# Kernel tuning notes

Measured on AMD Instinct MI355X. Metric: run time of the kernel, lower is better.

The kernel has to match this reference:

```python
import jax, jax.numpy as jnp
import numpy as np

B, I, O, E, K = 32768, 256, 128, 8, 4


def _layernorm(h, g, b, eps=1e-5):
    mu = h.mean(-1, keepdims=True)
    var = h.var(-1, keepdims=True)
    return (h - mu) * jax.lax.rsqrt(var + eps) * g + b


def setup_inputs():
    key = jax.random.key(0)
    ks = iter(jax.random.split(key, 40))
    def w(shape, scale=0.02):
        return jax.random.normal(next(ks), shape, dtype=jnp.float32) * scale
    inp = {
        'x': jax.random.normal(next(ks), (B, I), dtype=jnp.float32),
        'modality_id': jax.random.randint(next(ks), (B,), 0, 3, dtype=jnp.int32),
        # experts 0-1: Linear-ReLU-Linear (stacked over leading expert dim)
        'A_W1': w((2, O, I)), 'A_b1': w((2, O)), 'A_W2': w((2, O, O)), 'A_b2': w((2, O)),
        # experts 2-3: Linear-Tanh-BatchNorm1d(eval)-Linear
        'B_W1': w((2, O, I)), 'B_b1': w((2, O)),
        'B_g': jnp.ones((2, O), jnp.float32), 'B_be': jnp.zeros((2, O), jnp.float32),
        'B_W2': w((2, O, O)), 'B_b2': w((2, O)),
        # experts 4-5: Conv1d(1->4,k3,p1)-Flatten-Linear-GELU
        'C_cw': w((2, 4, 1, 3), 0.1), 'C_cb': w((2, 4)),
        'C_W': w((2, O, 4 * I)), 'C_b': w((2, O)),
        # experts 6-7: Linear-SiLU-LayerNorm-Linear
        'D_W1': w((2, O, I)), 'D_b1': w((2, O)),
        'D_g': jnp.ones((2, O), jnp.float32), 'D_be': jnp.zeros((2, O), jnp.float32),
        'D_W2': w((2, O, O)), 'D_b2': w((2, O)),
        # shared expert: Linear-ReLU-LayerNorm-Linear (dropout off in eval)
        'S_W1': w((O, I)), 'S_b1': w((O,)),
        'S_g': jnp.ones((O,), jnp.float32), 'S_be': jnp.zeros((O,), jnp.float32),
        'S_W2': w((O, O)), 'S_b2': w((O,)),
        # gate: Linear(I+1 -> I//2)-Tanh-Linear(-> E)
        'G_W1': w((I // 2, I + 1)), 'G_b1': w((I // 2,)),
        'G_W2': w((E, I // 2)), 'G_b2': w((E,)),
    }
    return inp


def _forward(x, modality_id, A_W1, A_b1, A_W2, A_b2, B_W1, B_b1, B_g, B_be, B_W2, B_b2,
             C_cw, C_cb, C_W, C_b, D_W1, D_b1, D_g, D_be, D_W2, D_b2,
             S_W1, S_b1, S_g, S_be, S_W2, S_b2, G_W1, G_b1, G_W2, G_b2):
    Bsz = x.shape[0]
    mod = modality_id.astype(x.dtype)[:, None]
    gate_in = jnp.concatenate([x, mod], axis=-1)                 # [B, I+1]
    gh = jnp.tanh(gate_in @ G_W1.T + G_b1)
    logits = jnp.clip((gh @ G_W2.T + G_b2) / 0.7, -10.0, 10.0)   # [B, E]
    topv, topi = jax.lax.top_k(logits, K)
    topw = jax.nn.softmax(topv, axis=-1)                          # [B, K]

    # experts 0-1
    hA = jax.nn.relu(jnp.einsum('bi,eoi->beo', x, A_W1) + A_b1)
    outA = jnp.einsum('beo,epo->bep', hA, A_W2) + A_b2
    # experts 2-3 (BatchNorm eval: running mean 0, var 1)
    hB = jnp.tanh(jnp.einsum('bi,eoi->beo', x, B_W1) + B_b1)
    hB = hB * jax.lax.rsqrt(jnp.asarray(1.0 + 1e-5, x.dtype)) * B_g + B_be
    outB = jnp.einsum('beo,epo->bep', hB, B_W2) + B_b2
    # experts 4-5
    xc = x[:, None, :]                                            # [B,1,I]
    outC = []
    for e in range(2):
        conv = jax.lax.conv_general_dilated(
            xc, C_cw[e], (1,), [(1, 1)],
            dimension_numbers=('NCH', 'OIH', 'NCH')) + C_cb[e][None, :, None]  # [B,4,I]
        flat = conv.reshape(Bsz, 4 * x.shape[1])
        outC.append(jax.nn.gelu(flat @ C_W[e].T + C_b[e], approximate=False))
    outC = jnp.stack(outC, axis=1)
    # experts 6-7
    hD = jax.nn.silu(jnp.einsum('bi,eoi->beo', x, D_W1) + D_b1)
    hD = _layernorm(hD, D_g, D_be)
    outD = jnp.einsum('beo,epo->bep', hD, D_W2) + D_b2

    expert_outputs = jnp.concatenate([outA, outB, outC, outD], axis=1)  # [B,E,O]
    picked = jnp.take_along_axis(expert_outputs, topi[:, :, None], axis=1)  # [B,K,O]
    private = jnp.sum(topw[:, :, None] * picked, axis=1)                # [B,O]

    hS = jax.nn.relu(x @ S_W1.T + S_b1)
    hS = _layernorm(hS, S_g, S_be)
    shared = hS @ S_W2.T + S_b2                                         # [B,O]

    usage = jax.nn.softmax(logits, axis=-1).mean(0)                     # [E]
    ideal = jnp.full_like(usage, 1.0 / E)
    # F.kl_div(log(usage+1e-10), ideal, reduction='batchmean') with N=E
    aux = jnp.mean(ideal * (jnp.log(ideal) - jnp.log(usage + 1e-10)))
    return shared, private, aux


def reference(x, modality_id, A_W1, A_b1, A_W2, A_b2, B_W1, B_b1, B_g, B_be, B_W2, B_b2,
              C_cw, C_cb, C_W, C_b, D_W1, D_b1, D_g, D_be, D_W2, D_b2,
              S_W1, S_b1, S_g, S_be, S_W2, S_b2, G_W1, G_b1, G_W2, G_b2):
    return _forward(x, modality_id, A_W1, A_b1, A_W2, A_b2, B_W1, B_b1, B_g, B_be, B_W2, B_b2,
                    C_cw, C_cb, C_W, C_b, D_W1, D_b1, D_g, D_be, D_W2, D_b2,
                    S_W1, S_b1, S_g, S_be, S_W2, S_b2, G_W1, G_b1, G_W2, G_b2)
```

## Files before the change

kernel.cpp:

```cpp
#include <hip/hip_runtime.h>
#include <hip/hip_bf16.h>
#include <math.h>

typedef __attribute__((ext_vector_type(8))) short short8;
typedef __attribute__((ext_vector_type(4))) float f32x4;
typedef __attribute__((ext_vector_type(4))) unsigned short us4;

#define MFMA16(a,b,c) __builtin_amdgcn_mfma_f32_16x16x32_bf16((a),(b),(c),0,0,0)

#define OFF_W1CAT   0u
#define OFF_W2CAT   589824u
#define OFF_B1      950272u
#define OFF_B2      954880u
#define OFF_LNG     958464u
#define OFF_LNB     960000u
#define OFF_BSC     961536u
#define OFF_BBI     962560u
#define OFF_USAGE   963584u
#define OFF_W8      963712u
#define OFF_W1T     2012288u
#define OFF_GW1HF   2143872u
#define OFF_GW1LF   2209408u
#define OFF_CNT     2274944u
#define OFF_LIST    2275008u

#define DELTA 3e-4f

__device__ __forceinline__ unsigned short f2bf(float f) {
  union { float f; unsigned u; } v; v.f = f;
  return (unsigned short)((v.u + 0x7fffu + ((v.u >> 16) & 1u)) >> 16);
}
__device__ __forceinline__ float bf2f(unsigned short b) {
  union { unsigned u; float f; } v; v.u = ((unsigned)b) << 16; return v.f;
}
__device__ __forceinline__ float frcp(float x) { return __builtin_amdgcn_rcpf(x); }
__device__ __forceinline__ float ftanh(float x) {
  float ax = fabsf(x);
  float t = __expf(-2.f * ax);
  float r = (1.f - t) * frcp(1.f + t);
  return copysignf(r, x);
}
__device__ __forceinline__ float ftanh_acc(float x) {
  float ax = fabsf(x);
  float t = __expf(-2.f * ax);
  float r = (1.f - t) / (1.f + t);
  return copysignf(r, x);
}
__device__ __forceinline__ float fsilu(float x) {
  return x * frcp(1.f + __expf(-x));
}
__device__ __forceinline__ float fgelu(float x) {
  float ax = fabsf(x) * 0.70710678118654752f;
  float t = frcp(fmaf(0.3275911f, ax, 1.f));
  float p = fmaf(t, 1.061405429f, -1.453152027f);
  p = fmaf(t, p, 1.421413741f);
  p = fmaf(t, p, -0.284496736f);
  p = fmaf(t, p, 0.254829592f);
  p *= t;
  float erfv = copysignf(fmaf(-p, __expf(-ax * ax), 1.f), x);
  return 0.5f * x * (1.f + erfv);
}
__device__ __forceinline__ void gld_lds16(const void* g, void* l) {
  __builtin_amdgcn_global_load_lds(
      (const __attribute__((address_space(1))) void*)g,
      (__attribute__((address_space(3))) void*)l, 16, 0, 0);
}

__global__ __launch_bounds__(256) void prep_kernel(
    const float* __restrict__ A_W1, const float* __restrict__ A_b1,
    const float* __restrict__ A_W2, const float* __restrict__ A_b2,
    const float* __restrict__ B_W1, const float* __restrict__ B_b1,
    const float* __restrict__ B_g,  const float* __restrict__ B_be,
    const float* __restrict__ B_W2, const float* __restrict__ B_b2,
    const float* __restrict__ C_cw, const float* __restrict__ C_cb,
    const float* __restrict__ C_W,  const float* __restrict__ C_b,
    const float* __restrict__ D_W1, const float* __restrict__ D_b1,
    const float* __restrict__ D_g,  const float* __restrict__ D_be,
    const float* __restrict__ D_W2, const float* __restrict__ D_b2,
    const float* __restrict__ S_W1, const float* __restrict__ S_b1,
    const float* __restrict__ S_g,  const float* __restrict__ S_be,
    const float* __restrict__ S_W2, const float* __restrict__ S_b2,
    const float* __restrict__ G_W1,
    unsigned short* __restrict__ W1cat, unsigned short* __restrict__ W2cat,
    float* __restrict__ W1T,
    unsigned short* __restrict__ GW1HF, unsigned short* __restrict__ GW1LF,
    float* __restrict__ b1cat, float* __restrict__ b2cat,
    float* __restrict__ lng, float* __restrict__ lnb,
    float* __restrict__ bsc, float* __restrict__ bbi,
    float* __restrict__ usage)
{
  int tid = blockIdx.x * 256 + threadIdx.x;
  if (tid < 294912) {
    int g = tid >> 15, rem = tid & 32767;
    int j = rem & 7, lane = (rem >> 3) & 63, nt = (rem >> 9) & 7, ks = rem >> 12;
    int p = nt * 16 + (lane & 15);
    int k = ks * 32 + (lane >> 4) * 8 + j;
    int src = p * 256 + k;
    float v;
    if (g < 2)      v = A_W1[g * 32768 + src];
    else if (g < 4) v = B_W1[(g - 2) * 32768 + src];
    else if (g < 6) {
      int e = g - 4;
      v = 0.f;
      for (int c = 0; c < 4; ++c)
        for (int jj = 0; jj < 3; ++jj) {
          int h = k + 1 - jj;
          if (h >= 0 && h < 256)
            v += C_cw[e*12 + c*3 + jj] * C_W[e*131072 + p*1024 + c*256 + h];
        }
    }
    else if (g < 8) v = D_W1[(g - 6) * 32768 + src];
    else            v = S_W1[src];
    W1cat[tid] = f2bf(v);
    return;
  }
  tid -= 294912;
  if (tid < 114688) {
    int g = tid >> 14, rem = tid & 16383;
    int j = rem & 7, lane = (rem >> 3) & 63, nt = (rem >> 9) & 7, ks = rem >> 12;
    int p = nt * 16 + (lane & 15);
    int k = ks * 32 + (lane >> 4) * 8 + j;
    int src = p * 128 + k;
    float v;
    if (g < 2)      v = A_W2[g * 16384 + src];
    else if (g < 4) v = B_W2[(g - 2) * 16384 + src];
    else if (g < 6) v = D_W2[(g - 4) * 16384 + src];
    else            v = S_W2[src];
    W2cat[tid] = f2bf(v);
    return;
  }
  tid -= 114688;
  if (tid < 32896) {
    int k = tid / 128, o = tid % 128;
    W1T[tid] = G_W1[o * 257 + k];
    return;
  }
  tid -= 32896;
  if (tid < 32768) {
    int j = tid & 7, lane = (tid >> 3) & 63, nt = (tid >> 9) & 7, ks = tid >> 12;
    int o = nt * 16 + (lane & 15);
    int k = ks * 32 + (lane >> 4) * 8 + j;
    float v = G_W1[o * 257 + k];
    unsigned short h = f2bf(v);
    GW1HF[tid] = h;
    GW1LF[tid] = f2bf(v - bf2f(h));
    return;
  }
  tid -= 32768;
  if (tid < 1152) {
    int g = tid / 128, p = tid % 128;
    float v;
    if (g < 2)      v = A_b1[tid];
    else if (g < 4) v = B_b1[p + (g - 2) * 128];
    else if (g < 6) v = C_b[(g - 4) * 128 + p];
    else if (g < 8) v = D_b1[p + (g - 6) * 128];
    else            v = S_b1[p];
    b1cat[tid] = v;
    return;
  }
  tid -= 1152;
  if (tid < 896) {
    int g = tid / 128, p = tid % 128;
    float v;
    if (g < 2)      v = A_b2[tid];
    else if (g < 4) v = B_b2[p + (g - 2) * 128];
    else if (g < 6) v = D_b2[p + (g - 4) * 128];
    else            v = S_b2[p];
    b2cat[tid] = v;
    return;
  }
  tid -= 896;
  if (tid < 768) {
    if (tid < 384) {
      int j = tid / 128, p = tid % 128;
      lng[tid] = (j < 2) ? D_g[tid] : S_g[p];
    } else {
      int q = tid - 384; int j = q / 128, p = q % 128;
      lnb[q] = (j < 2) ? D_be[q] : S_be[p];
    }
    return;
  }
  tid -= 768;
  if (tid < 512) {
    if (tid < 256) bsc[tid] = B_g[tid];
    else           bbi[tid - 256] = B_be[tid - 256];
    return;
  }
  tid -= 512;
  if (tid < 8) usage[tid] = 0.f;
}

__global__ __launch_bounds__(256) void prep2_kernel(
    const float* __restrict__ C_cw_unused, const float* __restrict__ C_cb,
    const float* __restrict__ C_W, float* __restrict__ b1cat, int* __restrict__ cnt)
{
  int tid = blockIdx.x * 256 + threadIdx.x;
  if (tid == 0) *cnt = 0;
  int e = tid >> 9, rem = tid & 511;
  int p = rem >> 2, c = rem & 3;
  const float4* row = (const float4*)(C_W + e*131072 + p*1024 + c*256);
  float s = 0.f;
  for (int q = 0; q < 64; ++q) {
    float4 v = row[q];
    s += v.x + v.y + v.z + v.w;
  }
  atomicAdd(&b1cat[(4 + e) * 128 + p], C_cb[e * 4 + c] * s);
}

__global__ __launch_bounds__(512, 4) void gate_fast_kernel(
    const float* __restrict__ x, const int* __restrict__ modality,
    const unsigned short* __restrict__ GW1HF, const unsigned short* __restrict__ GW1LF,
    const float* __restrict__ G_W1, const float* __restrict__ G_b1,
    const float* __restrict__ G_W2, const float* __restrict__ G_b2,
    float* __restrict__ w8full, float* __restrict__ usage,
    int* __restrict__ cnt, int* __restrict__ list)
{
  __shared__ float gh[64][132];
  __shared__ float lgs[64][9];
  const int tid = threadIdx.x;
  const int wv = tid >> 6, lane = tid & 63;
  const int l15 = lane & 15, l4 = lane >> 4;
  const int tg = wv >> 1, half = wv & 1;
  const int tb = blockIdx.x * 64;
  const int tw = tb + tg * 16;

  const short8* srcH = (const short8*)GW1HF;
  const short8* srcL = (const short8*)GW1LF;

  short8 XH[8], XL[8];
#pragma unroll
  for (int ks = 0; ks < 8; ++ks) {
    const float* xr = x + (size_t)(tw + l15) * 256 + ks * 32 + l4 * 8;
    float4 u = *(const float4*)xr, v = *(const float4*)(xr + 4);
    float xv[8] = {u.x, u.y, u.z, u.w, v.x, v.y, v.z, v.w};
    short8 hh, ll;
#pragma unroll
    for (int j2 = 0; j2 < 8; ++j2) {
      unsigned short h = f2bf(xv[j2]);
      hh[j2] = (short)h;
      ll[j2] = (short)f2bf(xv[j2] - bf2f(h));
    }
    XH[ks] = hh; XL[ks] = ll;
  }

  f32x4 zero = {0.f, 0.f, 0.f, 0.f};
  f32x4 acc[4];
#pragma unroll
  for (int n = 0; n < 4; ++n) acc[n] = zero;
#pragma unroll
  for (int ks = 0; ks < 8; ++ks) {
#pragma unroll
    for (int n = 0; n < 4; ++n) {
      int fi = ks * 512 + (half * 4 + n) * 64 + lane;
      short8 bh = srcH[fi];
      short8 bl = srcL[fi];
      acc[n] = MFMA16(XH[ks], bh, acc[n]);
      acc[n] = MFMA16(XH[ks], bl, acc[n]);
      acc[n] = MFMA16(XL[ks], bh, acc[n]);
    }
  }
  float mf[4];
#pragma unroll
  for (int r = 0; r < 4; ++r) mf[r] = (float)modality[tw + l4 * 4 + r];
#pragma unroll
  for (int n = 0; n < 4; ++n) {
    int o = (half * 4 + n) * 16 + l15;
    float wm = G_W1[o * 257 + 256];
    float b = G_b1[o];
#pragma unroll
    for (int r = 0; r < 4; ++r)
      gh[tg * 16 + l4 * 4 + r][o] = ftanh_acc(fmaf(mf[r], wm, acc[n][r]) + b);
  }
  __syncthreads();

  {
    int t2 = tid >> 3, e2 = tid & 7;
    float lg = 0.f;
    for (int o2 = 0; o2 < 128; ++o2)
      lg = fmaf(gh[t2][o2], G_W2[e2 * 128 + o2], lg);
    float s = (lg + G_b2[e2]) / 0.7f;
    lgs[t2][e2] = fminf(fmaxf(s, -10.f), 10.f);
  }
  __syncthreads();

  if (wv == 0) {
    int token = tb + lane;
    float v[8];
#pragma unroll
    for (int e = 0; e < 8; ++e) v[e] = lgs[lane][e];
    float tv[5]; int ti[5]; unsigned msk = 0;
    for (int kk = 0; kk < 5; ++kk) {
      float best = -1e30f; int bi = 0;
      for (int e = 0; e < 8; ++e)
        if (!((msk >> e) & 1u) && v[e] > best) { best = v[e]; bi = e; }
      tv[kk] = best; ti[kk] = bi; msk |= 1u << bi;
    }
    float uw[8];
#pragma unroll
    for (int e = 0; e < 8; ++e) uw[e] = 0.f;
    if (tv[3] - tv[4] < DELTA) {
      int idx = atomicAdd(cnt, 1);
      list[idx] = token;
    } else {
      float mx = tv[0], den = 0.f, wk4[4];
#pragma unroll
      for (int kk = 0; kk < 4; ++kk) { wk4[kk] = expf(tv[kk] - mx); den += wk4[kk]; }
#pragma unroll
      for (int e = 0; e < 8; ++e) {
        float val = 0.f;
#pragma unroll
        for (int kk = 0; kk < 4; ++kk) if (ti[kk] == e) val = wk4[kk] / den;
        w8full[(size_t)token * 8 + e] = val;
      }
      float dall = 0.f, pe[8];
#pragma unroll
      for (int e = 0; e < 8; ++e) { pe[e] = expf(v[e] - mx); dall += pe[e]; }
#pragma unroll
      for (int e = 0; e < 8; ++e) uw[e] = pe[e] / dall;
    }
    for (int m = 1; m <= 32; m <<= 1)
#pragma unroll
      for (int e = 0; e < 8; ++e) uw[e] += __shfl_xor(uw[e], m);
    if (lane == 0)
      for (int e = 0; e < 8; ++e) atomicAdd(usage + e, uw[e]);
  }
}

__global__ __launch_bounds__(256) void gate_slow_kernel(
    const float* __restrict__ x, const int* __restrict__ modality,
    const float* __restrict__ W1T, const float* __restrict__ G_b1,
    const float* __restrict__ G_W2, const float* __restrict__ G_b2,
    const int* __restrict__ cnt, const int* __restrict__ list,
    float* __restrict__ w8full, float* __restrict__ usage)
{
  __shared__ float w1l[32896];
  __shared__ float w2l[8][132];
  __shared__ float xs[4][2][256];
  __shared__ float gh[4][2][128];
  const int n = *cnt;
  if (blockIdx.x * 8 >= n) return;

  for (int idx = threadIdx.x; idx < 8224; idx += 256)
    ((float4*)w1l)[idx] = ((const float4*)W1T)[idx];
  for (int idx = threadIdx.x; idx < 1024; idx += 256)
    w2l[idx >> 7][idx & 127] = G_W2[idx];
  __syncthreads();

  const int wvl = threadIdx.x >> 6, lane = threadIdx.x & 63;
  for (int i0 = blockIdx.x * 8 + wvl * 2; i0 < n; i0 += 2048) {
    const bool v1 = (i0 + 1) < n;
    const int T0 = __builtin_amdgcn_readfirstlane(list[i0]);
    const int T1 = __builtin_amdgcn_readfirstlane(v1 ? list[i0 + 1] : list[i0]);
#pragma unroll
    for (int q = 0; q < 4; ++q) {
      xs[wvl][0][q * 64 + lane] = x[(size_t)T0 * 256 + q * 64 + lane];
      xs[wvl][1][q * 64 + lane] = x[(size_t)T1 * 256 + q * 64 + lane];
    }
    float a0 = 0.f, a1 = 0.f, c0 = 0.f, c1 = 0.f;
#pragma unroll 8
    for (int k = 0; k < 256; ++k) {
      float w0 = w1l[k * 128 + lane];
      float w1 = w1l[k * 128 + 64 + lane];
      float x0 = xs[wvl][0][k];
      float x1 = xs[wvl][1][k];
      a0 = fmaf(x0, w0, a0);
      a1 = fmaf(x0, w1, a1);
      c0 = fmaf(x1, w0, c0);
      c1 = fmaf(x1, w1, c1);
    }
    {
      float xm0 = (float)modality[T0];
      float xm1 = (float)modality[T1];
      float w0 = w1l[256 * 128 + lane];
      float w1 = w1l[256 * 128 + 64 + lane];
      a0 = fmaf(xm0, w0, a0);
      a1 = fmaf(xm0, w1, a1);
      c0 = fmaf(xm1, w0, c0);
      c1 = fmaf(xm1, w1, c1);
    }
    gh[wvl][0][lane]      = (float)tanh((double)(a0 + G_b1[lane]));
    gh[wvl][0][64 + lane] = (float)tanh((double)(a1 + G_b1[64 + lane]));
    gh[wvl][1][lane]      = (float)tanh((double)(c0 + G_b1[lane]));
    gh[wvl][1][64 + lane] = (float)tanh((double)(c1 + G_b1[64 + lane]));
    float lg = 0.f;
    if (lane < 16) {
      int tt2 = lane >> 3, ee = lane & 7;
      for (int o = 0; o < 128; ++o)
        lg = fmaf(gh[wvl][tt2][o], w2l[ee][o], lg);
    }
    float v[8];
#pragma unroll
    for (int e = 0; e < 8; ++e) v[e] = __shfl(lg, (lane & 8) + e);
    if (lane == 0 || (lane == 8 && v1)) {
      const int T = (lane == 0) ? T0 : T1;
#pragma unroll
      for (int e = 0; e < 8; ++e)
        v[e] = fminf(fmaxf((v[e] + G_b2[e]) / 0.7f, -10.f), 10.f);
      float tv[4]; int ti[4]; unsigned msk = 0;
      for (int kk = 0; kk < 4; ++kk) {
        float best = -1e30f; int bi = 0;
        for (int e = 0; e < 8; ++e)
          if (!((msk >> e) & 1u) && v[e] > best) { best = v[e]; bi = e; }
        tv[kk] = best; ti[kk] = bi; msk |= 1u << bi;
      }
      float mx = tv[0], den = 0.f, wk4[4];
#pragma unroll
      for (int kk = 0; kk < 4; ++kk) { wk4[kk] = expf(tv[kk] - mx); den += wk4[kk]; }
#pragma unroll
      for (int e = 0; e < 8; ++e) {
        float val = 0.f;
#pragma unroll
        for (int kk = 0; kk < 4; ++kk) if (ti[kk] == e) val = wk4[kk] / den;
        w8full[(size_t)T * 8 + e] = val;
      }
      float dall = 0.f, pe[8];
#pragma unroll
      for (int e = 0; e < 8; ++e) { pe[e] = expf(v[e] - mx); dall += pe[e]; }
      for (int e = 0; e < 8; ++e) atomicAdd(usage + e, pe[e] / dall);
    }
  }
}

__global__ __launch_bounds__(512, 2) void moe_kernel(
    const float* __restrict__ x,
    const unsigned short* __restrict__ W1cat, const unsigned short* __restrict__ W2cat,
    const float* __restrict__ b1cat, const float* __restrict__ b2cat,
    const float* __restrict__ lng, const float* __restrict__ lnb,
    const float* __restrict__ bsc, const float* __restrict__ bbi,
    const float* __restrict__ w8full, float* __restrict__ out)
{
  __shared__ unsigned char smem[131072];
  short8* W1L = (short8*)smem;
  short8* W2L = (short8*)(smem + 65536);
  unsigned char* HS = smem + 98304 + (threadIdx.x >> 6) * 4096;

  const int tid = threadIdx.x;
  const int wv = tid >> 6, lane = tid & 63;
  const int l15 = lane & 15, l4 = lane >> 4;
  const int tb = blockIdx.x * 128 + wv * 16;

  short8 A[8];
#pragma unroll
  for (int ks = 0; ks < 8; ++ks) {
    const float* xr = x + (size_t)(tb + l15) * 256 + ks * 32 + l4 * 8;
    float4 u = *(const float4*)xr, v = *(const float4*)(xr + 4);
    short8 a;
    a[0]=(short)f2bf(u.x); a[1]=(short)f2bf(u.y); a[2]=(short)f2bf(u.z); a[3]=(short)f2bf(u.w);
    a[4]=(short)f2bf(v.x); a[5]=(short)f2bf(v.y); a[6]=(short)f2bf(v.z); a[7]=(short)f2bf(v.w);
    A[ks] = a;
  }

  f32x4 zero = {0.f, 0.f, 0.f, 0.f};
  f32x4 pacc[8];
#pragma unroll
  for (int nt = 0; nt < 8; ++nt) pacc[nt] = zero;
  const float RS = 1.0f / sqrtf(1.0f + 1e-5f);

  for (int g = 0; g < 9; ++g) {
    const int type = (g < 2) ? 0 : (g < 4) ? 1 : (g < 6) ? 2 : (g < 8) ? 3 : 4;
    const int g2 = (g < 4) ? g : ((g == 8) ? 6 : g - 2);

    __syncthreads();
    {
      const char* W1g = (const char*)W1cat + (size_t)g * 65536;
      const char* W2g = (const char*)W2cat + (size_t)g2 * 32768;
      char* W1Lb = (char*)smem;
      char* W2Lb = (char*)smem + 65536;
      const int wb = wv * 1024;
#pragma unroll
      for (int i = 0; i < 8; ++i) {
        int off = i * 8192 + wb;
        gld_lds16(W1g + off + lane * 16, W1Lb + off);
      }
#pragma unroll
      for (int i = 0; i < 4; ++i) {
        int off = i * 8192 + wb;
        gld_lds16(W2g + off + lane * 16, W2Lb + off);
      }
      asm volatile("s_waitcnt vmcnt(0)" ::: "memory");
    }
    __syncthreads();

    f32x4 acc[8];
#pragma unroll
    for (int nt = 0; nt < 8; ++nt) acc[nt] = zero;
#pragma unroll
    for (int ks = 0; ks < 8; ++ks)
#pragma unroll
      for (int nt = 0; nt < 8; ++nt)
        acc[nt] = MFMA16(A[ks], W1L[(ks * 8 + nt) * 64 + lane], acc[nt]);

    const float* b1 = b1cat + g * 128;

    if (type == 2) {
#pragma unroll
      for (int r = 0; r < 4; ++r) {
        float wv_ = w8full[(size_t)(tb + l4 * 4 + r) * 8 + g];
#pragma unroll
        for (int nt = 0; nt < 8; ++nt) {
          float h = fgelu(acc[nt][r] + b1[nt * 16 + l15]);
          pacc[nt][r] += wv_ * h;
        }
      }
      continue;
    }
#pragma unroll
    for (int r = 0; r < 4; ++r)
#pragma unroll
      for (int nt = 0; nt < 8; ++nt) {
        float h = acc[nt][r] + b1[nt * 16 + l15];
        if (type == 0)      h = fmaxf(h, 0.f);
        else if (type == 1) {
          int col = (g - 2) * 128 + nt * 16 + l15;
          h = ftanh(h) * RS * bsc[col] + bbi[col];
        }
        else if (type == 3) h = fsilu(h);
        else                h = fmaxf(h, 0.f);
        acc[nt][r] = h;
      }
    if (type >= 3) {
      int li = (type == 4) ? 2 : (g - 6);
#pragma unroll
      for (int r = 0; r < 4; ++r) {
        float s1 = 0.f, s2 = 0.f;
#pragma unroll
        for (int nt = 0; nt < 8; ++nt) { float h = acc[nt][r]; s1 += h; s2 += h * h; }
        for (int m = 1; m <= 8; m <<= 1) { s1 += __shfl_xor(s1, m); s2 += __shfl_xor(s2, m); }
        float mu = s1 * (1.f / 128.f);
        float var = s2 * (1.f / 128.f) - mu * mu;
        float sc = __builtin_amdgcn_rsqf(var + 1e-5f);
#pragma unroll
        for (int nt = 0; nt < 8; ++nt) {
          int col = nt * 16 + l15;
          acc[nt][r] = (acc[nt][r] - mu) * sc * lng[li * 128 + col] + lnb[li * 128 + col];
        }
      }
    }
#pragma unroll
    for (int r = 0; r < 4; ++r) {
      int row = l4 * 4 + r;
#pragma unroll
      for (int nt = 0; nt < 8; ++nt) {
        int bytecol = (nt * 16 + l15) * 2;
        int addr = row * 256 + ((((bytecol >> 4) ^ (row & 7)) << 4) | (bytecol & 15));
        *(unsigned short*)(HS + addr) = f2bf(acc[nt][r]);
      }
    }
    short8 a2[4];
#pragma unroll
    for (int ks = 0; ks < 4; ++ks) {
      int ar = l15 * 256 + ((((ks * 4 + l4) ^ (l15 & 7)) << 4));
      a2[ks] = *(const short8*)(HS + ar);
    }
    f32x4 acc2[8];
#pragma unroll
    for (int nt = 0; nt < 8; ++nt) acc2[nt] = zero;
#pragma unroll
    for (int ks = 0; ks < 4; ++ks)
#pragma unroll
      for (int nt = 0; nt < 8; ++nt)
        acc2[nt] = MFMA16(a2[ks], W2L[(ks * 8 + nt) * 64 + lane], acc2[nt]);

    const float* b2 = b2cat + g2 * 128;
    if (type == 4) {
#pragma unroll
      for (int r = 0; r < 4; ++r) {
        int token = tb + l4 * 4 + r;
#pragma unroll
        for (int nt = 0; nt < 8; ++nt)
          out[(size_t)token * 128 + nt * 16 + l15] = acc2[nt][r] + b2[nt * 16 + l15];
      }
    } else {
#pragma unroll
      for (int r = 0; r < 4; ++r) {
        float wv_ = w8full[(size_t)(tb + l4 * 4 + r) * 8 + g];
#pragma unroll
        for (int nt = 0; nt < 8; ++nt)
          pacc[nt][r] += wv_ * (acc2[nt][r] + b2[nt * 16 + l15]);
      }
    }
  }
#pragma unroll
  for (int r = 0; r < 4; ++r) {
    int token = tb + l4 * 4 + r;
#pragma unroll
    for (int nt = 0; nt < 8; ++nt)
      out[4194304 + (size_t)token * 128 + nt * 16 + l15] = pacc[nt][r];
  }
}

__global__ void aux_kernel(const float* __restrict__ usage, float* __restrict__ out) {
  if (threadIdx.x == 0 && blockIdx.x == 0) {
    float a = 0.f;
    for (int e = 0; e < 8; ++e) {
      float u = usage[e] * (1.0f / 32768.0f);
      a += 0.125f * (logf(0.125f) - logf(u + 1e-10f));
    }
    out[8388608] = a * 0.125f;
  }
}

extern "C" void kernel_launch(void* const* d_in, const int* in_sizes, int n_in,
                              void* d_out, int out_size, void* d_ws, size_t ws_size,
                              hipStream_t stream) {
  (void)in_sizes; (void)n_in; (void)out_size; (void)ws_size;
  const float* x    = (const float*)d_in[0];
  const int*   mod  = (const int*)d_in[1];
  const float* A_W1 = (const float*)d_in[2];
  const float* A_b1 = (const float*)d_in[3];
  const float* A_W2 = (const float*)d_in[4];
  const float* A_b2 = (const float*)d_in[5];
  const float* B_W1 = (const float*)d_in[6];
  const float* B_b1 = (const float*)d_in[7];
  const float* B_g  = (const float*)d_in[8];
  const float* B_be = (const float*)d_in[9];
  const float* B_W2 = (const float*)d_in[10];
  const float* B_b2 = (const float*)d_in[11];
  const float* C_cw = (const float*)d_in[12];
  const float* C_cb = (const float*)d_in[13];
  const float* C_W  = (const float*)d_in[14];
  const float* C_b  = (const float*)d_in[15];
  const float* D_W1 = (const float*)d_in[16];
  const float* D_b1 = (const float*)d_in[17];
  const float* D_g  = (const float*)d_in[18];
  const float* D_be = (const float*)d_in[19];
  const float* D_W2 = (const float*)d_in[20];
  const float* D_b2 = (const float*)d_in[21];
  const float* S_W1 = (const float*)d_in[22];
  const float* S_b1 = (const float*)d_in[23];
  const float* S_g  = (const float*)d_in[24];
  const float* S_be = (const float*)d_in[25];
  const float* S_W2 = (const float*)d_in[26];
  const float* S_b2 = (const float*)d_in[27];
  const float* G_W1 = (const float*)d_in[28];
  const float* G_b1 = (const float*)d_in[29];
  const float* G_W2 = (const float*)d_in[30];
  const float* G_b2 = (const float*)d_in[31];

  char* ws = (char*)d_ws;
  unsigned short* W1cat = (unsigned short*)(ws + OFF_W1CAT);
  unsigned short* W2cat = (unsigned short*)(ws + OFF_W2CAT);
  float* W1T    = (float*)(ws + OFF_W1T);
  unsigned short* GW1HF = (unsigned short*)(ws + OFF_GW1HF);
  unsigned short* GW1LF = (unsigned short*)(ws + OFF_GW1LF);
  float* b1cat  = (float*)(ws + OFF_B1);
  float* b2cat  = (float*)(ws + OFF_B2);
  float* lng    = (float*)(ws + OFF_LNG);
  float* lnb    = (float*)(ws + OFF_LNB);
  float* bsc    = (float*)(ws + OFF_BSC);
  float* bbi    = (float*)(ws + OFF_BBI);
  float* usage  = (float*)(ws + OFF_USAGE);
  float* w8full = (float*)(ws + OFF_W8);
  int*   cnt    = (int*)(ws + OFF_CNT);
  int*   list   = (int*)(ws + OFF_LIST);
  float* out    = (float*)d_out;

  prep_kernel<<<1870, 256, 0, stream>>>(A_W1, A_b1, A_W2, A_b2, B_W1, B_b1, B_g, B_be,
      B_W2, B_b2, C_cw, C_cb, C_W, C_b, D_W1, D_b1, D_g, D_be, D_W2, D_b2,
      S_W1, S_b1, S_g, S_be, S_W2, S_b2, G_W1,
      W1cat, W2cat, W1T, GW1HF, GW1LF, b1cat, b2cat, lng, lnb, bsc, bbi, usage);
  prep2_kernel<<<4, 256, 0, stream>>>(C_cw, C_cb, C_W, b1cat, cnt);
  gate_fast_kernel<<<512, 512, 0, stream>>>(x, mod, GW1HF, GW1LF, G_W1, G_b1,
      G_W2, G_b2, w8full, usage, cnt, list);
  gate_slow_kernel<<<256, 256, 0, stream>>>(x, mod, W1T, G_b1, G_W2, G_b2,
      cnt, list, w8full, usage);
  moe_kernel<<<256, 512, 0, stream>>>(x, W1cat, W2cat, b1cat, b2cat, lng, lnb,
      bsc, bbi, w8full, out);
  aux_kernel<<<1, 64, 0, stream>>>(usage, out);
}
```

Before: 214.0 us.

## Split output columns across wave pairs and read W2 straight from global

Each block now handles 64 tokens instead of 128, and two waves share each 16-token tile by splitting the 128 output columns in half. The grid doubles to 512 blocks, and LDS use drops from 128KB to 80KB because W2 is no longer staged in shared memory and is read directly from global memory. The aim is more blocks per GPU and fewer registers per wave. The cost is extra block-wide barriers for the LayerNorm partial sums and for the hidden-tile exchange, plus W1 being staged twice as often per token overall.

```diff
diff --git a/kernel.cpp b/kernel.cpp
--- a/kernel.cpp
+++ b/kernel.cpp
@@ -429,15 +429,16 @@
     const float* __restrict__ bsc, const float* __restrict__ bbi,
     const float* __restrict__ w8full, float* __restrict__ out)
 {
-  __shared__ unsigned char smem[131072];
-  short8* W1L = (short8*)smem;
-  short8* W2L = (short8*)(smem + 65536);
-  unsigned char* HS = smem + 98304 + (threadIdx.x >> 6) * 4096;
-
+  __shared__ unsigned char smem[81920];
   const int tid = threadIdx.x;
   const int wv = tid >> 6, lane = tid & 63;
   const int l15 = lane & 15, l4 = lane >> 4;
-  const int tb = blockIdx.x * 128 + wv * 16;
+  const int t = wv >> 1, half = wv & 1;
+  const int tb = blockIdx.x * 64 + t * 16;
+  unsigned char* HS = smem + 65536 + t * 4096;
+  float* part = (float*)HS;
+  const short8* W1L = (const short8*)smem;
+  const short8* W2f = (const short8*)W2cat;
 
   short8 A[8];
 #pragma unroll
@@ -451,9 +452,9 @@
   }
 
   f32x4 zero = {0.f, 0.f, 0.f, 0.f};
-  f32x4 pacc[8];
-#pragma unroll
-  for (int nt = 0; nt < 8; ++nt) pacc[nt] = zero;
+  f32x4 pacc[4];
+#pragma unroll
+  for (int n = 0; n < 4; ++n) pacc[n] = zero;
   const float RS = 1.0f / sqrtf(1.0f + 1e-5f);
 
   for (int g = 0; g < 9; ++g) {
@@ -463,32 +464,23 @@
     __syncthreads();
     {
       const char* W1g = (const char*)W1cat + (size_t)g * 65536;
-      const char* W2g = (const char*)W2cat + (size_t)g2 * 32768;
-      char* W1Lb = (char*)smem;
-      char* W2Lb = (char*)smem + 65536;
-      const int wb = wv * 1024;
 #pragma unroll
       for (int i = 0; i < 8; ++i) {
-        int off = i * 8192 + wb;
-        gld_lds16(W1g + off + lane * 16, W1Lb + off);
-      }
-#pragma unroll
-      for (int i = 0; i < 4; ++i) {
-        int off = i * 8192 + wb;
-        gld_lds16(W2g + off + lane * 16, W2Lb + off);
+        int off = wv * 8192 + i * 1024;
+        gld_lds16(W1g + off + lane * 16, (char*)smem + off);
       }
       asm volatile("s_waitcnt vmcnt(0)" ::: "memory");
     }
     __syncthreads();
 
-    f32x4 acc[8];
-#pragma unroll
-    for (int nt = 0; nt < 8; ++nt) acc[nt] = zero;
+    f32x4 acc[4];
+#pragma unroll
+    for (int n = 0; n < 4; ++n) acc[n] = zero;
 #pragma unroll
     for (int ks = 0; ks < 8; ++ks)
 #pragma unroll
-      for (int nt = 0; nt < 8; ++nt)
-        acc[nt] = MFMA16(A[ks], W1L[(ks * 8 + nt) * 64 + lane], acc[nt]);
+      for (int n = 0; n < 4; ++n)
+        acc[n] = MFMA16(A[ks], W1L[(ks * 8 + half * 4 + n) * 64 + lane], acc[n]);
 
     const float* b1 = b1cat + g * 128;
 
@@ -497,9 +489,10 @@
       for (int r = 0; r < 4; ++r) {
         float wv_ = w8full[(size_t)(tb + l4 * 4 + r) * 8 + g];
 #pragma unroll
-        for (int nt = 0; nt < 8; ++nt) {
-          float h = fgelu(acc[nt][r] + b1[nt * 16 + l15]);
-          pacc[nt][r] += wv_ * h;
+        for (int n = 0; n < 4; ++n) {
+          int col = (half * 4 + n) * 16 + l15;
+          float h = fgelu(acc[n][r] + b1[col]);
+          pacc[n][r] += wv_ * h;
         }
       }
       continue;
@@ -507,59 +500,75 @@
 #pragma unroll
     for (int r = 0; r < 4; ++r)
 #pragma unroll
-      for (int nt = 0; nt < 8; ++nt) {
-        float h = acc[nt][r] + b1[nt * 16 + l15];
+      for (int n = 0; n < 4; ++n) {
+        int col = (half * 4 + n) * 16 + l15;
+        float h = acc[n][r] + b1[col];
         if (type == 0)      h = fmaxf(h, 0.f);
-        else if (type == 1) {
-          int col = (g - 2) * 128 + nt * 16 + l15;
-          h = ftanh(h) * RS * bsc[col] + bbi[col];
-        }
+        else if (type == 1) h = ftanh(h) * RS * bsc[(g - 2) * 128 + col] + bbi[(g - 2) * 128 + col];
         else if (type == 3) h = fsilu(h);
         else                h = fmaxf(h, 0.f);
-        acc[nt][r] = h;
+        acc[n][r] = h;
       }
     if (type >= 3) {
       int li = (type == 4) ? 2 : (g - 6);
+      float s1h[4], s2h[4];
 #pragma unroll
       for (int r = 0; r < 4; ++r) {
         float s1 = 0.f, s2 = 0.f;
 #pragma unroll
-        for (int nt = 0; nt < 8; ++nt) { float h = acc[nt][r]; s1 += h; s2 += h * h; }
+        for (int n = 0; n < 4; ++n) { float h = acc[n][r]; s1 += h; s2 += h * h; }
         for (int m = 1; m <= 8; m <<= 1) { s1 += __shfl_xor(s1, m); s2 += __shfl_xor(s2, m); }
+        s1h[r] = s1; s2h[r] = s2;
+      }
+      if (l15 == 0) {
+#pragma unroll
+        for (int r = 0; r < 4; ++r) {
+          part[half * 32 + (l4 * 4 + r)] = s1h[r];
+          part[half * 32 + 16 + (l4 * 4 + r)] = s2h[r];
+        }
+      }
+      __syncthreads();
+#pragma unroll
+      for (int r = 0; r < 4; ++r) {
+        int row = l4 * 4 + r;
+        float s1 = part[row] + part[32 + row];
+        float s2 = part[16 + row] + part[48 + row];
         float mu = s1 * (1.f / 128.f);
         float var = s2 * (1.f / 128.f) - mu * mu;
         float sc = __builtin_amdgcn_rsqf(var + 1e-5f);
 #pragma unroll
-        for (int nt = 0; nt < 8; ++nt) {
-          int col = nt * 16 + l15;
-          acc[nt][r] = (acc[nt][r] - mu) * sc * lng[li * 128 + col] + lnb[li * 128 + col];
+        for (int n = 0; n < 4; ++n) {
+          int col = (half * 4 + n) * 16 + l15;
+          acc[n][r] = (acc[n][r] - mu) * sc * lng[li * 128 + col] + lnb[li * 128 + col];
         }
       }
+      __syncthreads();
     }
 #pragma unroll
     for (int r = 0; r < 4; ++r) {
       int row = l4 * 4 + r;
 #pragma unroll
-      for (int nt = 0; nt < 8; ++nt) {
-        int bytecol = (nt * 16 + l15) * 2;
+      for (int n = 0; n < 4; ++n) {
+        int bytecol = ((half * 4 + n) * 16 + l15) * 2;
         int addr = row * 256 + ((((bytecol >> 4) ^ (row & 7)) << 4) | (bytecol & 15));
-        *(unsigned short*)(HS + addr) = f2bf(acc[nt][r]);
-      }
-    }
+        *(unsigned short*)(HS + addr) = f2bf(acc[n][r]);
+      }
+    }
+    __syncthreads();
     short8 a2[4];
 #pragma unroll
     for (int ks = 0; ks < 4; ++ks) {
       int ar = l15 * 256 + ((((ks * 4 + l4) ^ (l15 & 7)) << 4));
       a2[ks] = *(const short8*)(HS + ar);
     }
-    f32x4 acc2[8];
-#pragma unroll
-    for (int nt = 0; nt < 8; ++nt) acc2[nt] = zero;
+    f32x4 acc2[4];
+#pragma unroll
+    for (int n = 0; n < 4; ++n) acc2[n] = zero;
 #pragma unroll
     for (int ks = 0; ks < 4; ++ks)
 #pragma unroll
-      for (int nt = 0; nt < 8; ++nt)
-        acc2[nt] = MFMA16(a2[ks], W2L[(ks * 8 + nt) * 64 + lane], acc2[nt]);
+      for (int n = 0; n < 4; ++n)
+        acc2[n] = MFMA16(a2[ks], W2f[((size_t)(g2 * 4 + ks) * 8 + half * 4 + n) * 64 + lane], acc2[n]);
 
     const float* b2 = b2cat + g2 * 128;
     if (type == 4) {
@@ -567,16 +576,20 @@
       for (int r = 0; r < 4; ++r) {
         int token = tb + l4 * 4 + r;
 #pragma unroll
-        for (int nt = 0; nt < 8; ++nt)
-          out[(size_t)token * 128 + nt * 16 + l15] = acc2[nt][r] + b2[nt * 16 + l15];
+        for (int n = 0; n < 4; ++n) {
+          int col = (half * 4 + n) * 16 + l15;
+          out[(size_t)token * 128 + col] = acc2[n][r] + b2[col];
+        }
       }
     } else {
 #pragma unroll
       for (int r = 0; r < 4; ++r) {
         float wv_ = w8full[(size_t)(tb + l4 * 4 + r) * 8 + g];
 #pragma unroll
-        for (int nt = 0; nt < 8; ++nt)
-          pacc[nt][r] += wv_ * (acc2[nt][r] + b2[nt * 16 + l15]);
+        for (int n = 0; n < 4; ++n) {
+          int col = (half * 4 + n) * 16 + l15;
+          pacc[n][r] += wv_ * (acc2[n][r] + b2[col]);
+        }
       }
     }
   }
@@ -584,8 +597,10 @@
   for (int r = 0; r < 4; ++r) {
     int token = tb + l4 * 4 + r;
 #pragma unroll
-    for (int nt = 0; nt < 8; ++nt)
-      out[4194304 + (size_t)token * 128 + nt * 16 + l15] = pacc[nt][r];
+    for (int n = 0; n < 4; ++n) {
+      int col = (half * 4 + n) * 16 + l15;
+      out[4194304 + (size_t)token * 128 + col] = pacc[n][r];
+    }
   }
 }
 
@@ -664,7 +679,7 @@
       G_W2, G_b2, w8full, usage, cnt, list);
   gate_slow_kernel<<<256, 256, 0, stream>>>(x, mod, W1T, G_b1, G_W2, G_b2,
       cnt, list, w8full, usage);
-  moe_kernel<<<256, 512, 0, stream>>>(x, W1cat, W2cat, b1cat, b2cat, lng, lnb,
+  moe_kernel<<<512, 512, 0, stream>>>(x, W1cat, W2cat, b1cat, b2cat, lng, lnb,
       bsc, bbi, w8full, out);
   aux_kernel<<<1, 64, 0, stream>>>(usage, out);
 }
```

New measurement: 242.1 us. 13.1% more time.
